# Optimization experiments

Measured on AMD Instinct MI355X. Metric: run time of the kernel, lower is better.

## Reference

```python
import jax, jax.numpy as jnp
import numpy as np

B, T, C, H = 2, 2048, 1024, 16
N = C // H
TM_DIM, TD_DIM = 32, 64
EPS = 1e-5 * 8 ** 2  # GroupNorm eps from the module


def setup_inputs() -> dict:
    key = jax.random.key(0)
    ks = jax.random.split(key, 16)
    nrm = lambda k, shp, s: jax.random.normal(k, shp, dtype=jnp.float32) * s
    uni = lambda k, shp, a: jax.random.uniform(k, shp, jnp.float32, -a, a)
    ddd = (jnp.arange(C, dtype=jnp.float32) / C).reshape(1, 1, C)
    return {
        "x": nrm(ks[0], (B, T, C), 1.0),
        "time_maa_x": 1.0 - ddd ** 0.5,
        "time_maa_w": 1.0 - ddd ** 0.5,
        "time_maa_k": 1.0 - ddd ** 0.5,
        "time_maa_v": 1.0 - (ddd ** 0.5 + 0.15),
        "time_maa_r": 1.0 - ddd ** 0.25,
        "time_maa_g": 1.0 - ddd ** 0.25,
        "time_maa_w1": uni(ks[1], (C, 5 * TM_DIM), 1e-4),
        "time_maa_w2": uni(ks[2], (5, TM_DIM, C), 1e-4),
        "time_decay": jnp.linspace(-6.0, -1.0, C).astype(jnp.float32).reshape(1, 1, C),
        "time_decay_w1": uni(ks[3], (C, TD_DIM), 1e-4),
        "time_decay_w2": uni(ks[4], (TD_DIM, C), 1e-4),
        "time_faaaa": nrm(ks[5], (H, N), 0.1),
        "W_r": nrm(ks[6], (C, C), C ** -0.5),
        "W_k": nrm(ks[7], (C, C), C ** -0.5),
        "W_v": nrm(ks[8], (C, C), C ** -0.5),
        "W_g": nrm(ks[9], (C, C), C ** -0.5),
        "W_o": nrm(ks[10], (C, C), C ** -0.5),
        "ln_w": jnp.ones((C,), jnp.float32),
        "ln_b": jnp.zeros((C,), jnp.float32),
    }


def _forward(x, tmx, tmw, tmk, tmv, tmr, tmg, maa_w1, maa_w2, tdecay, td_w1,
             td_w2, u, Wr, Wk, Wv, Wg, Wo, ln_w, ln_b):
    Bq, Tq, Cq = x.shape
    # time_shift: x[t-1] with zero at t=0
    xx = jnp.concatenate([jnp.zeros_like(x[:, :1]), x[:, :-1]], axis=1) - x
    xxx = x + xx * tmx
    t5 = jnp.tanh(xxx @ maa_w1).reshape(Bq, Tq, 5, TM_DIM)
    m = jnp.einsum('btfe,fec->fbtc', t5, maa_w2)  # [5,B,T,C] data-dependent mix
    xw = x + xx * (tmw + m[0])
    xk = x + xx * (tmk + m[1])
    xv = x + xx * (tmv + m[2])
    xr = x + xx * (tmr + m[3])
    xg = x + xx * (tmg + m[4])
    r = xr @ Wr
    k = xk @ Wk
    v = xv @ Wv
    g = jax.nn.silu(xg @ Wg)
    w = tdecay + jnp.tanh(xw @ td_w1) @ td_w2          # [B,T,C] log-log decay
    decay = jnp.exp(-jnp.exp(w))                        # in (0,1)
    to_tbhn = lambda a: a.reshape(Bq, Tq, H, N).transpose(1, 0, 2, 3)
    rT, kT, vT, dT = (to_tbhn(a) for a in (r, k, v, decay))

    def step(S, inp):  # S: [B,H,N,N] (key_dim i, value_dim j)
        r_t, k_t, v_t, d_t = inp
        kv = k_t[..., :, None] * v_t[..., None, :]
        y = jnp.einsum('bhi,bhij->bhj', r_t, S + u[None, :, :, None] * kv)
        return d_t[..., None] * S + kv, y

    S0 = jnp.zeros((Bq, H, N, N), x.dtype)
    _, ys = jax.lax.scan(step, S0, (rT, kT, vT, dT))
    y = ys.transpose(1, 0, 2, 3).reshape(Bq, Tq, Cq)
    # GroupNorm with H groups over channels
    yh = y.reshape(Bq, Tq, H, N)
    mu = yh.mean(-1, keepdims=True)
    var = yh.var(-1, keepdims=True)
    yn = (yh - mu) / jnp.sqrt(var + EPS)
    yn = (yn * ln_w.reshape(H, N) + ln_b.reshape(H, N)).reshape(Bq, Tq, Cq)
    return (yn * g) @ Wo


def reference(x, time_maa_x, time_maa_w, time_maa_k, time_maa_v, time_maa_r,
              time_maa_g, time_maa_w1, time_maa_w2, time_decay, time_decay_w1,
              time_decay_w2, time_faaaa, W_r, W_k, W_v, W_g, W_o, ln_w, ln_b):
    return _forward(x, time_maa_x, time_maa_w, time_maa_k, time_maa_v,
                    time_maa_r, time_maa_g, time_maa_w1, time_maa_w2,
                    time_decay, time_decay_w1, time_decay_w2, time_faaaa,
                    W_r, W_k, W_v, W_g, W_o, ln_w, ln_b)
```

## Files before the change

### kernel.cpp

```cpp
#include <hip/hip_runtime.h>
#include <hip/hip_bf16.h>
#include <cstdint>
#include <cstddef>

#define B_ 2
#define T_ 2048
#define C_ 1024
#define H_ 16
#define NCH 32
#define CHL 64

typedef unsigned short ushort_t;
typedef __bf16 bf16x8 __attribute__((ext_vector_type(8)));
typedef float f32x4 __attribute__((ext_vector_type(4)));

__device__ __forceinline__ ushort_t f2bf(float f) {
  union { float f; uint32_t u; } x; x.f = f;
  uint32_t r = x.u + 0x7fffu + ((x.u >> 16) & 1u);
  return (ushort_t)(r >> 16);
}
__device__ __forceinline__ float bf2f(ushort_t h) {
  union { uint32_t u; float f; } x; x.u = (uint32_t)h << 16; return x.f;
}

__device__ __forceinline__ void gload16(const void* g, void* l) {
  __builtin_amdgcn_global_load_lds(
      (const __attribute__((address_space(1))) void*)g,
      (__attribute__((address_space(3))) void*)l, 16, 0, 0);
}

#define FENCE() asm volatile("" ::: "memory")
#define BAR() do { FENCE(); __builtin_amdgcn_s_barrier(); FENCE(); } while (0)

__device__ __forceinline__ void stb(ushort_t* tile, int row, int col, ushort_t v) {
  *(ushort_t*)((char*)tile + row * 128 + ((col * 2) ^ ((row & 7) << 4))) = v;
}
__device__ __forceinline__ bf16x8 ldb(const ushort_t* tile, int row, int kbyte) {
  return *(const bf16x8*)((const char*)tile + row * 128 + (kbyte ^ ((row & 7) << 4)));
}

struct TDesc { const float* src; ushort_t* dst; int R, Cc, Cpad; };
struct TArgs { TDesc d[9]; };

__global__ __launch_bounds__(256) void transpose_cvt(TArgs args) {
  TDesc D = args.d[blockIdx.z];
  int c0 = blockIdx.x * 32, r0 = blockIdx.y * 32;
  if (c0 >= D.Cpad || r0 >= D.R) return;
  __shared__ float tile[32][33];
  int tx = threadIdx.x & 31, ty = threadIdx.x >> 5;
#pragma unroll
  for (int i = 0; i < 32; i += 8) {
    int r = r0 + ty + i, c = c0 + tx;
    tile[ty + i][tx] = (r < D.R && c < D.Cc) ? D.src[(size_t)r * D.Cc + c] : 0.f;
  }
  __syncthreads();
#pragma unroll
  for (int i = 0; i < 32; i += 8) {
    int c = c0 + ty + i, r = r0 + tx;
    if (c < D.Cpad && r < D.R) D.dst[(size_t)c * D.R + r] = f2bf(tile[tx][ty + i]);
  }
}

__global__ __launch_bounds__(256) void prep_kernel(
    const float* __restrict__ x, const float* __restrict__ tmx,
    float* __restrict__ xx, ushort_t* __restrict__ xxx) {
  size_t idx = ((size_t)blockIdx.x * 256 + threadIdx.x) * 4;
  int tt = (int)((idx >> 10) & (T_ - 1));
  int c = (int)(idx & (C_ - 1));
  float4 xv = *(const float4*)&x[idx];
  float4 xp;
  if (tt == 0) { xp.x = xp.y = xp.z = xp.w = 0.f; }
  else xp = *(const float4*)&x[idx - C_];
  float4 tm = *(const float4*)&tmx[c];
  float4 d;
  d.x = xp.x - xv.x; d.y = xp.y - xv.y; d.z = xp.z - xv.z; d.w = xp.w - xv.w;
  *(float4*)&xx[idx] = d;
  xxx[idx + 0] = f2bf(xv.x + d.x * tm.x);
  xxx[idx + 1] = f2bf(xv.y + d.y * tm.y);
  xxx[idx + 2] = f2bf(xv.z + d.z * tm.z);
  xxx[idx + 3] = f2bf(xv.w + d.w * tm.w);
}

template <int EPI>
__global__ __launch_bounds__(256) void gemm_bt(
    const ushort_t* __restrict__ A, int lda,
    const ushort_t* __restrict__ Bt, int ldb,
    void* __restrict__ Cp, int ldc, int K,
    const float* __restrict__ aux2) {
  __shared__ ushort_t sA[128 * 32];
  __shared__ ushort_t sB[128 * 32];
  const int t = threadIdx.x;
  const int l = t & 63;
  const int w = t >> 6;
  const int wm = w >> 1, wn = w & 1;
  const int m0 = blockIdx.x * 128, n0 = blockIdx.y * 128;
  const int lr = l & 15;
  const int lk = (l >> 4) * 8;

  f32x4 acc[4][4] = {};

  for (int kt = 0; kt < K; kt += 32) {
    __syncthreads();
#pragma unroll
    for (int it = 0; it < 2; ++it) {
      int cbase = it * 256 + w * 64;
      int ca = cbase + l;
      int row = ca >> 2, kc = ca & 3;
      gload16(A + (size_t)(m0 + row) * lda + kt + kc * 8, (char*)sA + (size_t)cbase * 16);
      gload16(Bt + (size_t)(n0 + row) * ldb + kt + kc * 8, (char*)sB + (size_t)cbase * 16);
    }
    __syncthreads();
    bf16x8 af[4], bfr[4];
#pragma unroll
    for (int mi = 0; mi < 4; ++mi)
      af[mi] = *(const bf16x8*)&sA[(wm * 64 + mi * 16 + lr) * 32 + lk];
#pragma unroll
    for (int ni = 0; ni < 4; ++ni)
      bfr[ni] = *(const bf16x8*)&sB[(wn * 64 + ni * 16 + lr) * 32 + lk];
#pragma unroll
    for (int mi = 0; mi < 4; ++mi)
#pragma unroll
      for (int ni = 0; ni < 4; ++ni)
        acc[mi][ni] = __builtin_amdgcn_mfma_f32_16x16x32_bf16(af[mi], bfr[ni], acc[mi][ni], 0, 0, 0);
  }
#pragma unroll
  for (int mi = 0; mi < 4; ++mi) {
#pragma unroll
    for (int ni = 0; ni < 4; ++ni) {
      int col = n0 + wn * 64 + ni * 16 + lr;
#pragma unroll
      for (int r = 0; r < 4; ++r) {
        int row = m0 + wm * 64 + mi * 16 + (l >> 4) * 4 + r;
        float v = acc[mi][ni][r];
        size_t idx = (size_t)row * ldc + col;
        if constexpr (EPI == 0) {
          ((float*)Cp)[idx] = v;
        } else if constexpr (EPI == 4) {
          ((float*)Cp)[idx] = __expf(aux2[col] + v);
        }
      }
    }
  }
}

__global__ __launch_bounds__(256) void gemm_bt64(
    const ushort_t* __restrict__ A, int lda,
    const ushort_t* __restrict__ Bt, int ldb,
    ushort_t* __restrict__ Cp, int ldc, int K) {
  __shared__ ushort_t sA[64 * 32];
  __shared__ ushort_t sB[128 * 32];
  const int t = threadIdx.x;
  const int l = t & 63;
  const int w = t >> 6;
  const int m0 = blockIdx.x * 64, n0 = blockIdx.y * 128;
  const int lr = l & 15, lk = (l >> 4) * 8;

  f32x4 acc[4][2] = {};
  for (int kt = 0; kt < K; kt += 32) {
    __syncthreads();
    {
      int row = t >> 2, kc = t & 3;
      gload16(A + (size_t)(m0 + row) * lda + kt + kc * 8, (char*)sA + w * 1024);
    }
#pragma unroll
    for (int it = 0; it < 2; ++it) {
      int ca = it * 256 + t;
      int row = ca >> 2, kc = ca & 3;
      gload16(Bt + (size_t)(n0 + row) * ldb + kt + kc * 8,
              (char*)sB + it * 4096 + w * 1024);
    }
    __syncthreads();
    bf16x8 af[4], bfr[2];
#pragma unroll
    for (int mi = 0; mi < 4; ++mi)
      af[mi] = *(const bf16x8*)&sA[(mi * 16 + lr) * 32 + lk];
#pragma unroll
    for (int ni = 0; ni < 2; ++ni)
      bfr[ni] = *(const bf16x8*)&sB[(w * 32 + ni * 16 + lr) * 32 + lk];
#pragma unroll
    for (int mi = 0; mi < 4; ++mi)
#pragma unroll
      for (int ni = 0; ni < 2; ++ni)
        acc[mi][ni] = __builtin_amdgcn_mfma_f32_16x16x32_bf16(af[mi], bfr[ni], acc[mi][ni], 0, 0, 0);
  }
#pragma unroll
  for (int mi = 0; mi < 4; ++mi)
#pragma unroll
    for (int ni = 0; ni < 2; ++ni) {
      int col = n0 + w * 32 + ni * 16 + lr;
#pragma unroll
      for (int r = 0; r < 4; ++r) {
        int row = m0 + mi * 16 + (l >> 4) * 4 + r;
        Cp[(size_t)row * ldc + col] = f2bf(tanhf(acc[mi][ni][r]));
      }
    }
}

struct PDesc { const ushort_t* A; const ushort_t* Bt; float* C; int epi; };
struct PArgs { PDesc d[4]; };

__global__ __launch_bounds__(512, 1) void gemm_proj256(PArgs args) {
  PDesc D = args.d[blockIdx.z];
  __shared__ ushort_t sMem[2][2][4][4096];
  const int tid = threadIdx.x;
  const int w = tid >> 6, l = tid & 63;
  const int wm = w >> 2, wn = w & 3;
  const int lr = l & 15, hi4 = l >> 4;
  const int m0 = blockIdx.x * 256, n0 = blockIdx.y * 256;

  const int srow = tid >> 3;
  const int scol = (((tid & 7) ^ (srow & 7)) << 3);
  const ushort_t* Abase = D.A + (size_t)(m0 + srow) * C_ + scol;
  const ushort_t* Bbase = D.Bt + (size_t)(n0 + srow) * C_ + scol;
  const int dst16 = tid * 16;

  f32x4 acc[8][4] = {};
  bf16x8 bfr[2][4];

#define STG_A(db, unit, kt) \
  gload16(Abase + (size_t)(unit) * 64 * C_ + (kt), (char*)&sMem[db][0][unit][0] + dst16)
#define STG_B(db, unit, kt) \
  gload16(Bbase + (size_t)(unit) * 64 * C_ + (kt), (char*)&sMem[db][1][unit][0] + dst16)

#define LDA_(b, p, i, kk)                                                      \
  (*(const bf16x8*)((const char*)&sMem[b][0][wm * 2 + ((p) >> 1)][0] +         \
                    (((2 * (p) + (i)) & 3) * 16 + lr) * 128 +                  \
                    ((((kk)*4 + hi4) ^ (lr & 7)) << 4)))
#define LDB_(b, ni, kk)                                                        \
  (*(const bf16x8*)((const char*)&sMem[b][1][wn][0] +                          \
                    ((ni)*16 + lr) * 128 + ((((kk)*4 + hi4) ^ (lr & 7)) << 4)))

#define PH(b, p, STAGES, VM)                                                   \
  do {                                                                         \
    bf16x8 a00, a10, a01, a11;                                                 \
    if ((p) == 0) {                                                            \
      _Pragma("unroll") for (int kk = 0; kk < 2; ++kk)                         \
      _Pragma("unroll") for (int ni = 0; ni < 4; ++ni)                         \
        bfr[kk][ni] = LDB_(b, ni, kk);                                         \
    }                                                                          \
    a00 = LDA_(b, p, 0, 0); a10 = LDA_(b, p, 1, 0);                            \
    a01 = LDA_(b, p, 0, 1); a11 = LDA_(b, p, 1, 1);                            \
    STAGES;                                                                    \
    VM;                                                                        \
    BAR();                                                                     \
    asm volatile("s_waitcnt lgkmcnt(0)" ::: "memory");                         \
    __builtin_amdgcn_sched_barrier(0);                                         \
    __builtin_amdgcn_s_setprio(1);                                             \
    _Pragma("unroll") for (int ni = 0; ni < 4; ++ni) {                         \
      acc[2 * (p)][ni] = __builtin_amdgcn_mfma_f32_16x16x32_bf16(              \
          a00, bfr[0][ni], acc[2 * (p)][ni], 0, 0, 0);                         \
      acc[2 * (p) + 1][ni] = __builtin_amdgcn_mfma_f32_16x16x32_bf16(          \
          a10, bfr[0][ni], acc[2 * (p) + 1][ni], 0, 0, 0);                     \
      acc[2 * (p)][ni] = __builtin_amdgcn_mfma_f32_16x16x32_bf16(              \
          a01, bfr[1][ni], acc[2 * (p)][ni], 0, 0, 0);                         \
      acc[2 * (p) + 1][ni] = __builtin_amdgcn_mfma_f32_16x16x32_bf16(          \
          a11, bfr[1][ni], acc[2 * (p) + 1][ni], 0, 0, 0);                     \
    }                                                                          \
    __builtin_amdgcn_s_setprio(0);                                             \
    BAR();                                                                     \
  } while (0)

#define TILE(b, kt1, kt2)                                                      \
  do {                                                                         \
    PH(b, 0, { STG_A((b) ^ 1, 1, kt1); STG_A((b) ^ 1, 3, kt1); }, );           \
    PH(b, 1, { STG_B(b, 0, kt2); STG_B(b, 1, kt2); },                          \
       asm volatile("s_waitcnt vmcnt(10)" ::: "memory"));                      \
    PH(b, 2, { STG_B(b, 2, kt2); STG_B(b, 3, kt2); }, );                       \
    PH(b, 3, { STG_A(b, 0, kt2); STG_A(b, 2, kt2); },                          \
       asm volatile("s_waitcnt vmcnt(8)" ::: "memory"));                       \
  } while (0)

  STG_B(0, 0, 0);  STG_B(0, 1, 0);
  STG_B(0, 2, 0);  STG_B(0, 3, 0);
  STG_A(0, 0, 0);  STG_A(0, 2, 0);
  STG_A(0, 1, 0);  STG_A(0, 3, 0);
  STG_B(1, 0, 64); STG_B(1, 1, 64);
  STG_B(1, 2, 64); STG_B(1, 3, 64);
  STG_A(1, 0, 64); STG_A(1, 2, 64);
  asm volatile("s_waitcnt vmcnt(8)" ::: "memory");
  BAR();

#pragma unroll 1
  for (int j = 0; j < 16; j += 2) {
    int ka1 = ((j + 1) & 15) * 64, ka2 = ((j + 2) & 15) * 64;
    int kb1 = ((j + 2) & 15) * 64, kb2 = ((j + 3) & 15) * 64;
    TILE(0, ka1, ka2);
    TILE(1, kb1, kb2);
  }
  asm volatile("s_waitcnt vmcnt(0)" ::: "memory");

  const int epi = D.epi;
#pragma unroll
  for (int mi = 0; mi < 8; ++mi)
#pragma unroll
    for (int ni = 0; ni < 4; ++ni) {
      int col = n0 + wn * 64 + ni * 16 + lr;
#pragma unroll
      for (int r = 0; r < 4; ++r) {
        int row = m0 + wm * 128 + mi * 16 + hi4 * 4 + r;
        float v = acc[mi][ni][r];
        if (epi) v = v / (1.f + __expf(-v));
        D.C[(size_t)row * C_ + col] = v;
      }
    }
#undef TILE
#undef PH
#undef LDB_
#undef LDA_
#undef STG_B
#undef STG_A
}

struct MixArgs { const float* tm[5]; ushort_t* dst[5]; };

__global__ __launch_bounds__(256) void fused_mix(
    const float* __restrict__ x, const float* __restrict__ xx,
    const ushort_t* __restrict__ t5, const ushort_t* __restrict__ w2t,
    MixArgs margs) {
  __shared__ float xs[64 * 128];
  __shared__ float xxs[64 * 128];
  __shared__ ushort_t sA[64 * 32];
  __shared__ ushort_t sB[128 * 32];
  const int t = threadIdx.x;
  const int l = t & 63;
  const int w = t >> 6;
  const int wm = w >> 1, wn = w & 1;
  const int m0 = blockIdx.x * 64, n0 = blockIdx.y * 128;
  const int lr = l & 15;
  const int lk = (l >> 4) * 8;

#pragma unroll
  for (int it = 0; it < 8; ++it) {
    int row = it * 8 + (t >> 5);
    int c16 = t & 31;
    gload16(x + (size_t)(m0 + row) * C_ + n0 + c16 * 4, (char*)xs + row * 512 + c16 * 16);
    gload16(xx + (size_t)(m0 + row) * C_ + n0 + c16 * 4, (char*)xxs + row * 512 + c16 * 16);
  }

  for (int f = 0; f < 5; ++f) {
    __syncthreads();
    {
      int row = t >> 2, c8 = t & 3;
      gload16(t5 + (size_t)(m0 + row) * 256 + f * 32 + c8 * 8, (char*)sA + t * 16);
    }
#pragma unroll
    for (int it = 0; it < 2; ++it) {
      int row = it * 64 + (t >> 2), c8 = t & 3;
      gload16(w2t + (size_t)(n0 + row) * 160 + f * 32 + c8 * 8,
              (char*)sB + it * 4096 + t * 16);
    }
    __syncthreads();
    bf16x8 af[2], bfr[4];
#pragma unroll
    for (int mi = 0; mi < 2; ++mi)
      af[mi] = *(const bf16x8*)&sA[(wm * 32 + mi * 16 + lr) * 32 + lk];
#pragma unroll
    for (int ni = 0; ni < 4; ++ni)
      bfr[ni] = *(const bf16x8*)&sB[(wn * 64 + ni * 16 + lr) * 32 + lk];
    f32x4 acc[2][4] = {};
#pragma unroll
    for (int mi = 0; mi < 2; ++mi)
#pragma unroll
      for (int ni = 0; ni < 4; ++ni)
        acc[mi][ni] = __builtin_amdgcn_mfma_f32_16x16x32_bf16(af[mi], bfr[ni], acc[mi][ni], 0, 0, 0);
    const float* tmf = margs.tm[f];
    ushort_t* dst = margs.dst[f];
#pragma unroll
    for (int mi = 0; mi < 2; ++mi) {
#pragma unroll
      for (int ni = 0; ni < 4; ++ni) {
        int cl = wn * 64 + ni * 16 + lr;
        int col = n0 + cl;
        float tmv = tmf[col];
#pragma unroll
        for (int r = 0; r < 4; ++r) {
          int rl = wm * 32 + mi * 16 + (l >> 4) * 4 + r;
          int row = m0 + rl;
          float xv = xs[rl * 128 + cl];
          float xxv = xxs[rl * 128 + cl];
          dst[(size_t)row * C_ + col] = f2bf(xv + xxv * (tmv + acc[mi][ni][r]));
        }
      }
    }
  }
}

__global__ __launch_bounds__(256) void chunk_local(
    const float* __restrict__ rx, const float* __restrict__ kx,
    const float* __restrict__ vx, const float* __restrict__ lamx,
    const float* __restrict__ u, float* __restrict__ Mt,
    float* __restrict__ aLg, ushort_t* __restrict__ rAg,
    float* __restrict__ yo) {
  int c = blockIdx.x, bh = blockIdx.y;
  int b = bh >> 4, h = bh & 15;
  __shared__ ushort_t sRA[64 * 64], sKA[64 * 64], sKh[64 * 64], sKl[64 * 64],
                      sVh[64 * 64], sVl[64 * 64], sP[64 * 64];
  __shared__ float qsum[4][64];
  __shared__ float ruk[64];
  const int tid = threadIdx.x;
  const int i = tid & 63;
  const int q = tid >> 6;
  size_t base = ((size_t)b * T_ + (size_t)c * CHL) * C_ + h * 64;
  size_t cb = ((size_t)c * 32 + bh);

  float lam[16];
  float run = 0.f;
#pragma unroll
  for (int s = 0; s < 16; ++s) {
    lam[s] = lamx[base + (size_t)(q * 16 + s) * C_ + i];
    run += lam[s];
  }
  qsum[q][i] = run;
  __syncthreads();
  float pre = 0.f, ct = 0.f;
#pragma unroll
  for (int qq = 0; qq < 4; ++qq) {
    float vq = qsum[qq][i];
    ct += vq;
    if (qq < q) pre += vq;
  }
  float uu = u[h * 64 + i];
  float ci = pre;
#pragma unroll
  for (int s = 0; s < 16; ++s) {
    int t = q * 16 + s;
    ci += lam[s];
    float cl = ci - lam[s];
    size_t o = base + (size_t)t * C_ + i;
    float rv = rx[o], kv = kx[o], vv = vx[o];
    ushort_t ra = f2bf(rv * __expf(-cl));
    stb(sRA, t, i, ra);
    rAg[cb * 4096 + t * 64 + i] = ra;
    stb(sKA, t, i, f2bf(kv * __expf(ci)));
    float kal = kv * __expf(ci - ct);
    ushort_t khv = f2bf(kal);
    stb(sKh, i, t, khv);
    stb(sKl, i, t, f2bf(kal - bf2f(khv)));
    ushort_t vhv = f2bf(vv);
    stb(sVh, i, t, vhv);
    stb(sVl, i, t, f2bf(vv - bf2f(vhv)));
    float rr = rv * uu * kv;
#pragma unroll
    for (int m = 32; m; m >>= 1) rr += __shfl_xor(rr, m);
    if (i == 0) ruk[t] = rr;
  }
  if (q == 0) aLg[cb * 64 + i] = __expf(-ct);
  __syncthreads();

  const int l = tid & 63, w = tid >> 6;
  const int wm = w >> 1, wn = w & 1;
  const int lr = l & 15, hi4 = l >> 4;

  {
    f32x4 accP[2][2] = {};
#pragma unroll
    for (int kk = 0; kk < 2; ++kk) {
      bf16x8 af[2], bf_[2];
#pragma unroll
      for (int mi = 0; mi < 2; ++mi) af[mi] = ldb(sRA, wm * 32 + mi * 16 + lr, kk * 64 + hi4 * 16);
#pragma unroll
      for (int ni = 0; ni < 2; ++ni) bf_[ni] = ldb(sKA, wn * 32 + ni * 16 + lr, kk * 64 + hi4 * 16);
#pragma unroll
      for (int mi = 0; mi < 2; ++mi)
#pragma unroll
        for (int ni = 0; ni < 2; ++ni)
          accP[mi][ni] = __builtin_amdgcn_mfma_f32_16x16x32_bf16(af[mi], bf_[ni], accP[mi][ni], 0, 0, 0);
    }
#pragma unroll
    for (int mi = 0; mi < 2; ++mi)
#pragma unroll
      for (int ni = 0; ni < 2; ++ni)
#pragma unroll
        for (int r = 0; r < 4; ++r) {
          int tl = wm * 32 + mi * 16 + hi4 * 4 + r, sl = wn * 32 + ni * 16 + lr;
          float v = accP[mi][ni][r];
          v = sl < tl ? v : (sl == tl ? ruk[tl] : 0.f);
          stb(sP, tl, sl, f2bf(v));
        }
  }
  __syncthreads();

  f32x4 accY[2][2] = {}, accM[2][2] = {};
#pragma unroll
  for (int kk = 0; kk < 2; ++kk) {
    bf16x8 pa[2], vhA[2], vlA[2], vhB[2], vlB[2], khB[2], klB[2];
#pragma unroll
    for (int mi = 0; mi < 2; ++mi) {
      int rw = wm * 32 + mi * 16 + lr;
      pa[mi] = ldb(sP, rw, kk * 64 + hi4 * 16);
      vhA[mi] = ldb(sVh, rw, kk * 64 + hi4 * 16);
      vlA[mi] = ldb(sVl, rw, kk * 64 + hi4 * 16);
    }
#pragma unroll
    for (int ni = 0; ni < 2; ++ni) {
      int rw = wn * 32 + ni * 16 + lr;
      vhB[ni] = ldb(sVh, rw, kk * 64 + hi4 * 16);
      vlB[ni] = ldb(sVl, rw, kk * 64 + hi4 * 16);
      khB[ni] = ldb(sKh, rw, kk * 64 + hi4 * 16);
      klB[ni] = ldb(sKl, rw, kk * 64 + hi4 * 16);
    }
#pragma unroll
    for (int mi = 0; mi < 2; ++mi)
#pragma unroll
      for (int ni = 0; ni < 2; ++ni) {
        accY[mi][ni] = __builtin_amdgcn_mfma_f32_16x16x32_bf16(pa[mi], vhB[ni], accY[mi][ni], 0, 0, 0);
        accY[mi][ni] = __builtin_amdgcn_mfma_f32_16x16x32_bf16(pa[mi], vlB[ni], accY[mi][ni], 0, 0, 0);
        accM[mi][ni] = __builtin_amdgcn_mfma_f32_16x16x32_bf16(vhA[mi], khB[ni], accM[mi][ni], 0, 0, 0);
        accM[mi][ni] = __builtin_amdgcn_mfma_f32_16x16x32_bf16(vhA[mi], klB[ni], accM[mi][ni], 0, 0, 0);
        accM[mi][ni] = __builtin_amdgcn_mfma_f32_16x16x32_bf16(vlA[mi], khB[ni], accM[mi][ni], 0, 0, 0);
      }
  }
#pragma unroll
  for (int mi = 0; mi < 2; ++mi)
#pragma unroll
    for (int ni = 0; ni < 2; ++ni)
#pragma unroll
      for (int r = 0; r < 4; ++r) {
        int rw = wm * 32 + mi * 16 + hi4 * 4 + r;
        int cw = wn * 32 + ni * 16 + lr;
        yo[base + (size_t)rw * C_ + cw] = accY[mi][ni][r];
        Mt[cb * 4096 + rw * 64 + cw] = accM[mi][ni][r];
      }
}

__global__ __launch_bounds__(256) void combine2(
    const float* __restrict__ Mt, const float* __restrict__ aLg,
    ushort_t* __restrict__ S0h, ushort_t* __restrict__ S0l) {
  int bh = blockIdx.x >> 2;
  int ij = ((blockIdx.x & 3) * 256 + threadIdx.x) * 4;
  int i = ij & 63;
  float4 s = {0.f, 0.f, 0.f, 0.f};
  for (int c = 0; c < NCH; ++c) {
    size_t o = ((size_t)c * 32 + bh) * 4096 + ij;
    float4 m = *(const float4*)&Mt[o];
    float4 p = *(const float4*)&aLg[((size_t)c * 32 + bh) * 64 + i];
    ushort4 hi, lo;
    hi.x = f2bf(s.x); lo.x = f2bf(s.x - bf2f(hi.x));
    hi.y = f2bf(s.y); lo.y = f2bf(s.y - bf2f(hi.y));
    hi.z = f2bf(s.z); lo.z = f2bf(s.z - bf2f(hi.z));
    hi.w = f2bf(s.w); lo.w = f2bf(s.w - bf2f(hi.w));
    *(ushort4*)&S0h[o] = hi;
    *(ushort4*)&S0l[o] = lo;
    s.x = p.x * s.x + m.x; s.y = p.y * s.y + m.y;
    s.z = p.z * s.z + m.z; s.w = p.w * s.w + m.w;
  }
}

__global__ __launch_bounds__(256) void inter_gn(
    const ushort_t* __restrict__ rAg, const ushort_t* __restrict__ S0h,
    const ushort_t* __restrict__ S0l, const float* __restrict__ yin,
    const float* __restrict__ gx, const float* __restrict__ lnw,
    const float* __restrict__ lnb, ushort_t* __restrict__ Z) {
  int c = blockIdx.x, bh = blockIdx.y;
  int b = bh >> 4, h = bh & 15;
  __shared__ ushort_t sRA[64 * 64], sSh[64 * 64], sSl[64 * 64];
  __shared__ float st[64][2][2];
  const int tid = threadIdx.x;
  size_t cb = ((size_t)c * 32 + bh) * 4096;
#pragma unroll
  for (int it = 0; it < 2; ++it) {
    int lb = tid * 32 + it * 16;
    int row = lb >> 7, wi = lb & 127;
    int so = row * 128 + (wi ^ ((row & 7) << 4));
    *(uint4*)((char*)sRA + so) = *(const uint4*)((const char*)(rAg + cb) + lb);
    *(uint4*)((char*)sSh + so) = *(const uint4*)((const char*)(S0h + cb) + lb);
    *(uint4*)((char*)sSl + so) = *(const uint4*)((const char*)(S0l + cb) + lb);
  }
  const int l = tid & 63, w = tid >> 6;
  const int wm = w >> 1, wn = w & 1;
  const int lr = l & 15, hi4 = l >> 4;
  size_t base = ((size_t)b * T_ + (size_t)c * CHL) * C_ + h * 64;

  f32x4 acc[2][2];
#pragma unroll
  for (int mi = 0; mi < 2; ++mi)
#pragma unroll
    for (int ni = 0; ni < 2; ++ni)
#pragma unroll
      for (int r = 0; r < 4; ++r)
        acc[mi][ni][r] = yin[base + (size_t)(wm * 32 + mi * 16 + hi4 * 4 + r) * C_ +
                             wn * 32 + ni * 16 + lr];
  __syncthreads();
#pragma unroll
  for (int kk = 0; kk < 2; ++kk) {
    bf16x8 af[2], bh_[2], bl_[2];
#pragma unroll
    for (int mi = 0; mi < 2; ++mi) af[mi] = ldb(sRA, wm * 32 + mi * 16 + lr, kk * 64 + hi4 * 16);
#pragma unroll
    for (int ni = 0; ni < 2; ++ni) {
      bh_[ni] = ldb(sSh, wn * 32 + ni * 16 + lr, kk * 64 + hi4 * 16);
      bl_[ni] = ldb(sSl, wn * 32 + ni * 16 + lr, kk * 64 + hi4 * 16);
    }
#pragma unroll
    for (int mi = 0; mi < 2; ++mi)
#pragma unroll
      for (int ni = 0; ni < 2; ++ni) {
        acc[mi][ni] = __builtin_amdgcn_mfma_f32_16x16x32_bf16(af[mi], bh_[ni], acc[mi][ni], 0, 0, 0);
        acc[mi][ni] = __builtin_amdgcn_mfma_f32_16x16x32_bf16(af[mi], bl_[ni], acc[mi][ni], 0, 0, 0);
      }
  }
#pragma unroll
  for (int mi = 0; mi < 2; ++mi)
#pragma unroll
    for (int r = 0; r < 4; ++r) {
      int row = wm * 32 + mi * 16 + hi4 * 4 + r;
      float s1 = acc[mi][0][r] + acc[mi][1][r];
      float s2 = acc[mi][0][r] * acc[mi][0][r] + acc[mi][1][r] * acc[mi][1][r];
#pragma unroll
      for (int m = 1; m < 16; m <<= 1) { s1 += __shfl_xor(s1, m); s2 += __shfl_xor(s2, m); }
      if (lr == 0) { st[row][wn][0] = s1; st[row][wn][1] = s2; }
    }
  __syncthreads();
#pragma unroll
  for (int mi = 0; mi < 2; ++mi)
#pragma unroll
    for (int ni = 0; ni < 2; ++ni)
#pragma unroll
      for (int r = 0; r < 4; ++r) {
        int row = wm * 32 + mi * 16 + hi4 * 4 + r;
        int jl = wn * 32 + ni * 16 + lr;
        float S1 = st[row][0][0] + st[row][1][0];
        float S2 = st[row][0][1] + st[row][1][1];
        float mu = S1 * (1.f / 64.f);
        float var = S2 * (1.f / 64.f) - mu * mu;
        float rs = rsqrtf(var + 6.4e-4f);
        int col = h * 64 + jl;
        size_t o = base + (size_t)row * C_ + jl;
        float yn = (acc[mi][ni][r] - mu) * rs * lnw[col] + lnb[col];
        Z[o] = f2bf(yn * gx[o]);
      }
}

extern "C" void kernel_launch(void* const* d_in, const int* in_sizes, int n_in,
                              void* d_out, int out_size, void* d_ws, size_t ws_size,
                              hipStream_t stream) {
  const float* x    = (const float*)d_in[0];
  const float* tmx  = (const float*)d_in[1];
  const float* tmw  = (const float*)d_in[2];
  const float* tmk  = (const float*)d_in[3];
  const float* tmv  = (const float*)d_in[4];
  const float* tmr  = (const float*)d_in[5];
  const float* tmg  = (const float*)d_in[6];
  const float* maaw1 = (const float*)d_in[7];
  const float* maaw2 = (const float*)d_in[8];
  const float* tdec = (const float*)d_in[9];
  const float* tdw1 = (const float*)d_in[10];
  const float* tdw2 = (const float*)d_in[11];
  const float* u    = (const float*)d_in[12];
  const float* Wr   = (const float*)d_in[13];
  const float* Wk   = (const float*)d_in[14];
  const float* Wv   = (const float*)d_in[15];
  const float* Wg   = (const float*)d_in[16];
  const float* Wo   = (const float*)d_in[17];
  const float* lnw  = (const float*)d_in[18];
  const float* lnb  = (const float*)d_in[19];

  char* ws = (char*)d_ws;
  const size_t MB = 1ull << 20;
  float*    xx     = (float*)(ws + 0);
  ushort_t* xxx    = (ushort_t*)(ws + 16 * MB);
  ushort_t* WrT    = (ushort_t*)(ws + 24 * MB);
  ushort_t* WkT    = (ushort_t*)(ws + 26 * MB);
  ushort_t* WvT    = (ushort_t*)(ws + 28 * MB);
  ushort_t* WgT    = (ushort_t*)(ws + 30 * MB);
  ushort_t* WoT    = (ushort_t*)(ws + 32 * MB);
  ushort_t* maaW1T = (ushort_t*)(ws + 34 * MB);
  ushort_t* tdW1T  = (ushort_t*)(ws + 35 * MB);
  ushort_t* tdW2T  = (ushort_t*)(ws + 35 * MB + 256 * 1024);
  ushort_t* maaW2T = (ushort_t*)(ws + 35 * MB + 512 * 1024);
  ushort_t* t5     = (ushort_t*)(ws + 36 * MB);
  ushort_t* t5d    = (ushort_t*)(ws + 38 * MB);
  ushort_t* Xm[5];
  for (int f = 0; f < 5; ++f) Xm[f] = (ushort_t*)(ws + 40 * MB + (size_t)f * 8 * MB);
  float*    Mtb = (float*)(ws + 40 * MB);
  ushort_t* S0h = (ushort_t*)(ws + 56 * MB);
  ushort_t* S0l = (ushort_t*)(ws + 64 * MB);
  ushort_t* rAg = (ushort_t*)(ws + 72 * MB);
  float* rb   = (float*)(ws + 80 * MB);
  float* kb   = (float*)(ws + 96 * MB);
  float* vb   = (float*)(ws + 112 * MB);
  float* gb   = (float*)(ws + 128 * MB);
  float* lam  = (float*)(ws + 144 * MB);
  float* aLg  = (float*)(ws + 160 * MB);
  float* yb   = (float*)(ws + 0);
  ushort_t* Zb = (ushort_t*)(ws + 16 * MB);

  TArgs ta;
  ta.d[0] = TDesc{Wr,    WrT,    1024, 1024, 1024};
  ta.d[1] = TDesc{Wk,    WkT,    1024, 1024, 1024};
  ta.d[2] = TDesc{Wv,    WvT,    1024, 1024, 1024};
  ta.d[3] = TDesc{Wg,    WgT,    1024, 1024, 1024};
  ta.d[4] = TDesc{Wo,    WoT,    1024, 1024, 1024};
  ta.d[5] = TDesc{maaw1, maaW1T, 1024, 160,  256};
  ta.d[6] = TDesc{tdw1,  tdW1T,  1024, 64,   128};
  ta.d[7] = TDesc{tdw2,  tdW2T,  64,   1024, 1024};
  ta.d[8] = TDesc{maaw2, maaW2T, 160,  1024, 1024};
  transpose_cvt<<<dim3(32, 32, 9), 256, 0, stream>>>(ta);

  prep_kernel<<<(B_ * T_ * C_) / 1024, 256, 0, stream>>>(x, tmx, xx, xxx);

  gemm_bt64<<<dim3(64, 2), 256, 0, stream>>>(xxx, C_, maaW1T, C_, t5, 256, C_);

  MixArgs ma;
  ma.tm[0] = tmw; ma.tm[1] = tmk; ma.tm[2] = tmv; ma.tm[3] = tmr; ma.tm[4] = tmg;
  for (int f = 0; f < 5; ++f) ma.dst[f] = Xm[f];
  fused_mix<<<dim3(64, 8), 256, 0, stream>>>(x, xx, t5, maaW2T, ma);

  PArgs pa;
  pa.d[0] = PDesc{Xm[3], WrT, rb, 0};
  pa.d[1] = PDesc{Xm[1], WkT, kb, 0};
  pa.d[2] = PDesc{Xm[2], WvT, vb, 0};
  pa.d[3] = PDesc{Xm[4], WgT, gb, 1};
  gemm_proj256<<<dim3(16, 4, 4), 512, 0, stream>>>(pa);

  gemm_bt64<<<dim3(64, 1), 256, 0, stream>>>(Xm[0], C_, tdW1T, C_, t5d, 128, C_);
  gemm_bt<4><<<dim3(32, 8), 256, 0, stream>>>(t5d, 128, tdW2T, 64, lam, C_, 64, tdec);

  chunk_local<<<dim3(NCH, B_ * H_), 256, 0, stream>>>(rb, kb, vb, lam, u, Mtb, aLg, rAg, yb);
  combine2<<<128, 256, 0, stream>>>(Mtb, aLg, S0h, S0l);
  inter_gn<<<dim3(NCH, B_ * H_), 256, 0, stream>>>(rAg, S0h, S0l, yb, gb, lnw, lnb, Zb);

  gemm_bt<0><<<dim3(32, 8), 256, 0, stream>>>(Zb, C_, WoT, C_, (float*)d_out, C_, C_, nullptr);
}
```

Measured before the change: 210.4 us.

## Halve small GEMM M-tile, store gate in bf16, reuse 256-tile GEMM for output

The tanh low-rank GEMMs now use 32-row tiles, which doubles the grid from 128 or 64 blocks so more compute units are busy. The silu gate output is written as bf16 instead of fp32, roughly halving its write and its later read in inter_gn, at some cost in precision. The final output projection switches from the 128x128 gemm_bt to the 256x256 gemm_proj256 kernel with a single z-slice, giving more data reuse per block but only 64 blocks.

```diff
diff --git a/kernel.cpp b/kernel.cpp
--- a/kernel.cpp
+++ b/kernel.cpp
@@ -133,34 +133,34 @@
         int row = m0 + wm * 64 + mi * 16 + (l >> 4) * 4 + r;
         float v = acc[mi][ni][r];
         size_t idx = (size_t)row * ldc + col;
-        if constexpr (EPI == 0) {
+        if constexpr (EPI == 4) {
+          ((float*)Cp)[idx] = __expf(aux2[col] + v);
+        } else {
           ((float*)Cp)[idx] = v;
-        } else if constexpr (EPI == 4) {
-          ((float*)Cp)[idx] = __expf(aux2[col] + v);
         }
       }
     }
   }
 }
 
-__global__ __launch_bounds__(256) void gemm_bt64(
+__global__ __launch_bounds__(256) void gemm_bt32(
     const ushort_t* __restrict__ A, int lda,
     const ushort_t* __restrict__ Bt, int ldb,
     ushort_t* __restrict__ Cp, int ldc, int K) {
-  __shared__ ushort_t sA[64 * 32];
+  __shared__ ushort_t sA[32 * 32];
   __shared__ ushort_t sB[128 * 32];
   const int t = threadIdx.x;
   const int l = t & 63;
   const int w = t >> 6;
-  const int m0 = blockIdx.x * 64, n0 = blockIdx.y * 128;
+  const int m0 = blockIdx.x * 32, n0 = blockIdx.y * 128;
   const int lr = l & 15, lk = (l >> 4) * 8;
 
-  f32x4 acc[4][2] = {};
+  f32x4 acc[2][2] = {};
   for (int kt = 0; kt < K; kt += 32) {
     __syncthreads();
-    {
+    if (t < 128) {
       int row = t >> 2, kc = t & 3;
-      gload16(A + (size_t)(m0 + row) * lda + kt + kc * 8, (char*)sA + w * 1024);
+      gload16(A + (size_t)(m0 + row) * lda + kt + kc * 8, (char*)sA + t * 16);
     }
 #pragma unroll
     for (int it = 0; it < 2; ++it) {
@@ -170,21 +170,21 @@
               (char*)sB + it * 4096 + w * 1024);
     }
     __syncthreads();
-    bf16x8 af[4], bfr[2];
-#pragma unroll
-    for (int mi = 0; mi < 4; ++mi)
+    bf16x8 af[2], bfr[2];
+#pragma unroll
+    for (int mi = 0; mi < 2; ++mi)
       af[mi] = *(const bf16x8*)&sA[(mi * 16 + lr) * 32 + lk];
 #pragma unroll
     for (int ni = 0; ni < 2; ++ni)
       bfr[ni] = *(const bf16x8*)&sB[(w * 32 + ni * 16 + lr) * 32 + lk];
 #pragma unroll
-    for (int mi = 0; mi < 4; ++mi)
+    for (int mi = 0; mi < 2; ++mi)
 #pragma unroll
       for (int ni = 0; ni < 2; ++ni)
         acc[mi][ni] = __builtin_amdgcn_mfma_f32_16x16x32_bf16(af[mi], bfr[ni], acc[mi][ni], 0, 0, 0);
   }
 #pragma unroll
-  for (int mi = 0; mi < 4; ++mi)
+  for (int mi = 0; mi < 2; ++mi)
 #pragma unroll
     for (int ni = 0; ni < 2; ++ni) {
       int col = n0 + w * 32 + ni * 16 + lr;
@@ -196,7 +196,7 @@
     }
 }
 
-struct PDesc { const ushort_t* A; const ushort_t* Bt; float* C; int epi; };
+struct PDesc { const ushort_t* A; const ushort_t* Bt; void* C; int epi; };
 struct PArgs { PDesc d[4]; };
 
 __global__ __launch_bounds__(512, 1) void gemm_proj256(PArgs args) {
@@ -299,8 +299,13 @@
       for (int r = 0; r < 4; ++r) {
         int row = m0 + wm * 128 + mi * 16 + hi4 * 4 + r;
         float v = acc[mi][ni][r];
-        if (epi) v = v / (1.f + __expf(-v));
-        D.C[(size_t)row * C_ + col] = v;
+        size_t idx = (size_t)row * C_ + col;
+        if (epi == 2) {
+          v = v / (1.f + __expf(-v));
+          ((ushort_t*)D.C)[idx] = f2bf(v);
+        } else {
+          ((float*)D.C)[idx] = v;
+        }
       }
     }
 #undef TILE
@@ -549,7 +554,7 @@
 __global__ __launch_bounds__(256) void inter_gn(
     const ushort_t* __restrict__ rAg, const ushort_t* __restrict__ S0h,
     const ushort_t* __restrict__ S0l, const float* __restrict__ yin,
-    const float* __restrict__ gx, const float* __restrict__ lnw,
+    const ushort_t* __restrict__ gx, const float* __restrict__ lnw,
     const float* __restrict__ lnb, ushort_t* __restrict__ Z) {
   int c = blockIdx.x, bh = blockIdx.y;
   int b = bh >> 4, h = bh & 15;
@@ -627,7 +632,7 @@
         int col = h * 64 + jl;
         size_t o = base + (size_t)row * C_ + jl;
         float yn = (acc[mi][ni][r] - mu) * rs * lnw[col] + lnb[col];
-        Z[o] = f2bf(yn * gx[o]);
+        Z[o] = f2bf(yn * bf2f(gx[o]));
       }
 }
 
@@ -679,7 +684,7 @@
   float* rb   = (float*)(ws + 80 * MB);
   float* kb   = (float*)(ws + 96 * MB);
   float* vb   = (float*)(ws + 112 * MB);
-  float* gb   = (float*)(ws + 128 * MB);
+  ushort_t* gbh = (ushort_t*)(ws + 128 * MB);
   float* lam  = (float*)(ws + 144 * MB);
   float* aLg  = (float*)(ws + 160 * MB);
   float* yb   = (float*)(ws + 0);
@@ -699,7 +704,7 @@
 
   prep_kernel<<<(B_ * T_ * C_) / 1024, 256, 0, stream>>>(x, tmx, xx, xxx);
 
-  gemm_bt64<<<dim3(64, 2), 256, 0, stream>>>(xxx, C_, maaW1T, C_, t5, 256, C_);
+  gemm_bt32<<<dim3(128, 2), 256, 0, stream>>>(xxx, C_, maaW1T, C_, t5, 256, C_);
 
   MixArgs ma;
   ma.tm[0] = tmw; ma.tm[1] = tmk; ma.tm[2] = tmv; ma.tm[3] = tmr; ma.tm[4] = tmg;
@@ -710,15 +715,18 @@
   pa.d[0] = PDesc{Xm[3], WrT, rb, 0};
   pa.d[1] = PDesc{Xm[1], WkT, kb, 0};
   pa.d[2] = PDesc{Xm[2], WvT, vb, 0};
-  pa.d[3] = PDesc{Xm[4], WgT, gb, 1};
+  pa.d[3] = PDesc{Xm[4], WgT, gbh, 2};
   gemm_proj256<<<dim3(16, 4, 4), 512, 0, stream>>>(pa);
 
-  gemm_bt64<<<dim3(64, 1), 256, 0, stream>>>(Xm[0], C_, tdW1T, C_, t5d, 128, C_);
+  gemm_bt32<<<dim3(128, 1), 256, 0, stream>>>(Xm[0], C_, tdW1T, C_, t5d, 128, C_);
   gemm_bt<4><<<dim3(32, 8), 256, 0, stream>>>(t5d, 128, tdW2T, 64, lam, C_, 64, tdec);
 
   chunk_local<<<dim3(NCH, B_ * H_), 256, 0, stream>>>(rb, kb, vb, lam, u, Mtb, aLg, rAg, yb);
   combine2<<<128, 256, 0, stream>>>(Mtb, aLg, S0h, S0l);
-  inter_gn<<<dim3(NCH, B_ * H_), 256, 0, stream>>>(rAg, S0h, S0l, yb, gb, lnw, lnb, Zb);
-
-  gemm_bt<0><<<dim3(32, 8), 256, 0, stream>>>(Zb, C_, WoT, C_, (float*)d_out, C_, C_, nullptr);
-}
+  inter_gn<<<dim3(NCH, B_ * H_), 256, 0, stream>>>(rAg, S0h, S0l, yb, gbh, lnw, lnb, Zb);
+
+  PArgs po;
+  po.d[0] = PDesc{Zb, WoT, d_out, 0};
+  po.d[1] = po.d[0]; po.d[2] = po.d[0]; po.d[3] = po.d[0];
+  gemm_proj256<<<dim3(16, 4, 1), 512, 0, stream>>>(po);
+}
```

Measured after the change: 205.1 us. 1.03x faster.
